# Kernel tuning notes

Measured on AMD Instinct MI355X. Metric: run time of the kernel, lower is better.

Reference implementation:

```python
import jax, jax.numpy as jnp
import numpy as np

B, W, K = 262144, 8, 3      # batch of triples, context window, negatives per item
V, E = 100000, 128          # vocab, embedding dim


def setup_inputs() -> dict:
    key = jax.random.key(0)
    k1, k2, k3, k4, k5 = jax.random.split(key, 5)
    targets = jax.random.randint(k1, (B,), 0, V)
    contexts = jax.random.randint(k2, (B, W), 0, V)
    negsamples = jax.random.randint(k3, (B, K), 0, V)
    # learned params (small random so the loss/grads are non-degenerate)
    target_W = jax.random.normal(k4, (V, E), dtype=jnp.float32) * 0.01
    context_W = jax.random.normal(k5, (V, E), dtype=jnp.float32) * 0.01
    return {"targets": targets, "contexts": contexts, "negsamples": negsamples,
            "target_W": target_W, "context_W": context_W}


def reference(targets, contexts, negsamples, target_W, context_W):
    tgt = target_W[targets]                      # [B,E] one target embedding per triple
    ctx = context_W[contexts].mean(axis=1)       # [B,E] mean of context window embeddings
    neg = context_W[negsamples]                  # [B,K,E] negative-sample context embeddings
    pos_score = jnp.einsum('be,be->b', ctx, tgt)             # [B]
    neg_score = -jnp.einsum('bke,be->b', neg, tgt)           # [B] sum_k dot(-neg_k, tgt)
    per_item = jax.nn.log_sigmoid(pos_score) + jax.nn.log_sigmoid(neg_score)
    return -per_item.mean()                      # scalar NEG loss (sum over items / B)
```

## Files before the change

kernel.cpp:

```cpp
#include <hip/hip_runtime.h>
#include <math.h>
#include <stdint.h>

#define B_ITEMS 262144
#define W_CTX   8
#define K_NEG   3
#define E_DIM   128
#define V_VOCAB 100000

typedef _Float16 half_t;
typedef __attribute__((ext_vector_type(2))) _Float16 half2_t;

#define F16_TABLE_BYTES ((size_t)V_VOCAB * E_DIM * 2)

__device__ __forceinline__ float log_sigmoid_f(float x) {
    return fminf(x, 0.0f) - log1pf(expf(-fabsf(x)));
}

__device__ __forceinline__ float dot2acc(half2_t a, half2_t b, float c) {
#if __has_builtin(__builtin_amdgcn_fdot2)
    return __builtin_amdgcn_fdot2(a, b, c, false);
#else
    return c + (float)a[0] * (float)b[0] + (float)a[1] * (float)b[1];
#endif
}

__device__ __forceinline__ half2_t h2_from_u32(uint32_t u) {
    return __builtin_bit_cast(half2_t, u);
}
__device__ __forceinline__ uint32_t u32_from_h2(half2_t h) {
    return __builtin_bit_cast(uint32_t, h);
}

__global__ void init_out_kernel(float* out) {
    if (threadIdx.x == 0 && blockIdx.x == 0) out[0] = 0.0f;
}

__global__ void __launch_bounds__(256) convert_f16_both_kernel(
    const float* __restrict__ srcA, uint2* __restrict__ dstA,
    const float* __restrict__ srcB, uint2* __restrict__ dstB, int n4)
{
    int i = blockIdx.x * blockDim.x + threadIdx.x;
    const int stride = gridDim.x * blockDim.x;
    const float4* a4 = reinterpret_cast<const float4*>(srcA);
    const float4* b4 = reinterpret_cast<const float4*>(srcB);
    for (; i < n4; i += stride) {
        float4 va = a4[i];
        uint2 oa;
        oa.x = u32_from_h2(half2_t{(half_t)va.x, (half_t)va.y});
        oa.y = u32_from_h2(half2_t{(half_t)va.z, (half_t)va.w});
        dstA[i] = oa;
        if (dstB) {
            float4 vb = b4[i];
            uint2 ob;
            ob.x = u32_from_h2(half2_t{(half_t)vb.x, (half_t)vb.y});
            ob.y = u32_from_h2(half2_t{(half_t)vb.z, (half_t)vb.w});
            dstB[i] = ob;
        }
    }
}

template <bool CTX16, bool TGT16>
__global__ void __launch_bounds__(256, 8) cbow_kernel(
    const int*      __restrict__ targets,
    const int*      __restrict__ contexts,
    const int*      __restrict__ negsamples,
    const float*    __restrict__ target_W,
    const float*    __restrict__ context_W,
    const uint32_t* __restrict__ ctx16,
    const uint32_t* __restrict__ tgt16,
    float*          __restrict__ out)
{
    const int lane = threadIdx.x & 63;
    const int wib  = threadIdx.x >> 6;
    const int wid  = blockIdx.x * (blockDim.x >> 6) + wib;
    const int grp  = lane >> 4;
    const int sub  = lane & 15;
    const uint32_t sub16 = (uint32_t)sub * 16;

    const char* ctxb = reinterpret_cast<const char*>(ctx16);
    const char* tgtb = reinterpret_cast<const char*>(tgt16);

    float wave_sum = 0.0f;

    for (int i = 0; i < 8; ++i) {
        const int b = (wid * 8 + i) * 4 + grp;

        const int4 c0 = *reinterpret_cast<const int4*>(&contexts[b * W_CTX]);
        const int4 c1 = *reinterpret_cast<const int4*>(&contexts[b * W_CTX + 4]);
        const int  n0 = negsamples[b * K_NEG + 0];
        const int  n1 = negsamples[b * K_NEG + 1];
        const int  n2 = negsamples[b * K_NEG + 2];
        const int  t  = targets[b];

        half2_t tg[4];
        if constexpr (TGT16) {
            const uint4 tv = *reinterpret_cast<const uint4*>(
                tgtb + (((uint32_t)t) << 8) + sub16);
            tg[0] = h2_from_u32(tv.x); tg[1] = h2_from_u32(tv.y);
            tg[2] = h2_from_u32(tv.z); tg[3] = h2_from_u32(tv.w);
        } else {
            const float4 f0 = *reinterpret_cast<const float4*>(
                &target_W[(size_t)t * E_DIM + sub * 8]);
            const float4 f1 = *reinterpret_cast<const float4*>(
                &target_W[(size_t)t * E_DIM + sub * 8 + 4]);
            tg[0] = half2_t{(half_t)f0.x, (half_t)f0.y};
            tg[1] = half2_t{(half_t)f0.z, (half_t)f0.w};
            tg[2] = half2_t{(half_t)f1.x, (half_t)f1.y};
            tg[3] = half2_t{(half_t)f1.z, (half_t)f1.w};
        }

        float p0 = 0.f, p1 = 0.f, p2 = 0.f, p3 = 0.f;
        float q0 = 0.f, q1 = 0.f, q2 = 0.f, q3 = 0.f;

        auto row = [&](int idx, float& a0, float& a1, float& a2, float& a3) {
            if constexpr (CTX16) {
                const uint4 rv = *reinterpret_cast<const uint4*>(
                    ctxb + (((uint32_t)idx) << 8) + sub16);
                a0 = dot2acc(h2_from_u32(rv.x), tg[0], a0);
                a1 = dot2acc(h2_from_u32(rv.y), tg[1], a1);
                a2 = dot2acc(h2_from_u32(rv.z), tg[2], a2);
                a3 = dot2acc(h2_from_u32(rv.w), tg[3], a3);
            } else {
                const float4 f0 = *reinterpret_cast<const float4*>(
                    &context_W[(size_t)idx * E_DIM + sub * 8]);
                const float4 f1 = *reinterpret_cast<const float4*>(
                    &context_W[(size_t)idx * E_DIM + sub * 8 + 4]);
                a0 = dot2acc(half2_t{(half_t)f0.x, (half_t)f0.y}, tg[0], a0);
                a1 = dot2acc(half2_t{(half_t)f0.z, (half_t)f0.w}, tg[1], a1);
                a2 = dot2acc(half2_t{(half_t)f1.x, (half_t)f1.y}, tg[2], a2);
                a3 = dot2acc(half2_t{(half_t)f1.z, (half_t)f1.w}, tg[3], a3);
            }
        };

        row(c0.x, p0, p1, p2, p3);
        row(c0.y, p0, p1, p2, p3);
        row(c0.z, p0, p1, p2, p3);
        row(c0.w, p0, p1, p2, p3);
        row(c1.x, p0, p1, p2, p3);
        row(c1.y, p0, p1, p2, p3);
        row(c1.z, p0, p1, p2, p3);
        row(c1.w, p0, p1, p2, p3);
        row(n0,   q0, q1, q2, q3);
        row(n1,   q0, q1, q2, q3);
        row(n2,   q0, q1, q2, q3);

        float pos = (p0 + p1) + (p2 + p3);
        float neg = (q0 + q1) + (q2 + q3);

        #pragma unroll
        for (int off = 8; off > 0; off >>= 1) {
            pos += __shfl_xor(pos, off, 64);
            neg += __shfl_xor(neg, off, 64);
        }

        wave_sum += log_sigmoid_f(pos * (1.0f / W_CTX)) + log_sigmoid_f(-neg);
    }

    wave_sum += __shfl_xor(wave_sum, 16, 64);
    wave_sum += __shfl_xor(wave_sum, 32, 64);

    __shared__ float sm[4];
    if (lane == 0) sm[wib] = wave_sum;
    __syncthreads();
    if (threadIdx.x == 0) {
        atomicAdd(out, (sm[0] + sm[1] + sm[2] + sm[3]) * (-1.0f / (float)B_ITEMS));
    }
}

extern "C" void kernel_launch(void* const* d_in, const int* in_sizes, int n_in,
                              void* d_out, int out_size, void* d_ws, size_t ws_size,
                              hipStream_t stream) {
    const int*   targets    = (const int*)  d_in[0];
    const int*   contexts   = (const int*)  d_in[1];
    const int*   negsamples = (const int*)  d_in[2];
    const float* target_W   = (const float*)d_in[3];
    const float* context_W  = (const float*)d_in[4];
    float*       out        = (float*)      d_out;

    init_out_kernel<<<1, 64, 0, stream>>>(out);

    uint32_t* ctx16 = (uint32_t*)d_ws;
    uint32_t* tgt16 = (uint32_t*)((char*)d_ws + F16_TABLE_BYTES);
    const int n4 = V_VOCAB * E_DIM / 4;

    if (ws_size >= 2 * F16_TABLE_BYTES) {
        convert_f16_both_kernel<<<2048, 256, 0, stream>>>(
            context_W, (uint2*)ctx16, target_W, (uint2*)tgt16, n4);
        cbow_kernel<true, true><<<2048, 256, 0, stream>>>(
            targets, contexts, negsamples, target_W, context_W, ctx16, tgt16, out);
    } else if (ws_size >= F16_TABLE_BYTES) {
        convert_f16_both_kernel<<<2048, 256, 0, stream>>>(
            context_W, (uint2*)ctx16, nullptr, (uint2*)nullptr, n4);
        cbow_kernel<true, false><<<2048, 256, 0, stream>>>(
            targets, contexts, negsamples, target_W, context_W, ctx16, nullptr, out);
    } else {
        cbow_kernel<false, false><<<2048, 256, 0, stream>>>(
            targets, contexts, negsamples, target_W, context_W, nullptr, nullptr, out);
    }
}
```

Before: 240.9 us.

## Store context table as FP8 and gather half-size rows in the CBOW kernel

```diff
diff --git a/kernel.cpp b/kernel.cpp
--- a/kernel.cpp
+++ b/kernel.cpp
@@ -10,21 +10,21 @@
 
 typedef _Float16 half_t;
 typedef __attribute__((ext_vector_type(2))) _Float16 half2_t;
-
+typedef __attribute__((ext_vector_type(2))) float   fvec2;
+
+#define CTX_FP8_BYTES ((size_t)V_VOCAB * E_DIM)
 #define F16_TABLE_BYTES ((size_t)V_VOCAB * E_DIM * 2)
+
+#if __has_builtin(__builtin_amdgcn_cvt_pk_f32_fp8) && __has_builtin(__builtin_amdgcn_cvt_pk_fp8_f32)
+#define HAVE_FP8 1
+#else
+#define HAVE_FP8 0
+#endif
 
 __device__ __forceinline__ float log_sigmoid_f(float x) {
     return fminf(x, 0.0f) - log1pf(expf(-fabsf(x)));
 }
 
-__device__ __forceinline__ float dot2acc(half2_t a, half2_t b, float c) {
-#if __has_builtin(__builtin_amdgcn_fdot2)
-    return __builtin_amdgcn_fdot2(a, b, c, false);
-#else
-    return c + (float)a[0] * (float)b[0] + (float)a[1] * (float)b[1];
-#endif
-}
-
 __device__ __forceinline__ half2_t h2_from_u32(uint32_t u) {
     return __builtin_bit_cast(half2_t, u);
 }
@@ -36,10 +36,41 @@
     if (threadIdx.x == 0 && blockIdx.x == 0) out[0] = 0.0f;
 }
 
+#if HAVE_FP8
+__global__ void __launch_bounds__(256) convert_fp8_kernel(
+    const float* __restrict__ ctx, uint2* __restrict__ ctx8,
+    const float* __restrict__ tgt, uint4* __restrict__ tgt16,
+    int n8, float* __restrict__ out)
+{
+    if (blockIdx.x == 0 && threadIdx.x == 0) out[0] = 0.0f;
+    int i = blockIdx.x * blockDim.x + threadIdx.x;
+    const int stride = gridDim.x * blockDim.x;
+    const float4* c4 = reinterpret_cast<const float4*>(ctx);
+    const float4* t4 = reinterpret_cast<const float4*>(tgt);
+    for (; i < n8; i += stride) {
+        float4 a = c4[2 * i], b = c4[2 * i + 1];
+        int lo = __builtin_amdgcn_cvt_pk_fp8_f32(a.x, a.y, 0, false);
+        lo     = __builtin_amdgcn_cvt_pk_fp8_f32(a.z, a.w, lo, true);
+        int hi = __builtin_amdgcn_cvt_pk_fp8_f32(b.x, b.y, 0, false);
+        hi     = __builtin_amdgcn_cvt_pk_fp8_f32(b.z, b.w, hi, true);
+        ctx8[i] = make_uint2((uint32_t)lo, (uint32_t)hi);
+        float4 ta = t4[2 * i], tb = t4[2 * i + 1];
+        uint4 o;
+        o.x = u32_from_h2(half2_t{(half_t)ta.x, (half_t)ta.y});
+        o.y = u32_from_h2(half2_t{(half_t)ta.z, (half_t)ta.w});
+        o.z = u32_from_h2(half2_t{(half_t)tb.x, (half_t)tb.y});
+        o.w = u32_from_h2(half2_t{(half_t)tb.z, (half_t)tb.w});
+        tgt16[i] = o;
+    }
+}
+#endif
+
 __global__ void __launch_bounds__(256) convert_f16_both_kernel(
     const float* __restrict__ srcA, uint2* __restrict__ dstA,
-    const float* __restrict__ srcB, uint2* __restrict__ dstB, int n4)
+    const float* __restrict__ srcB, uint2* __restrict__ dstB,
+    int n4, float* __restrict__ out)
 {
+    if (blockIdx.x == 0 && threadIdx.x == 0) out[0] = 0.0f;
     int i = blockIdx.x * blockDim.x + threadIdx.x;
     const int stride = gridDim.x * blockDim.x;
     const float4* a4 = reinterpret_cast<const float4*>(srcA);
@@ -50,25 +81,24 @@
         oa.x = u32_from_h2(half2_t{(half_t)va.x, (half_t)va.y});
         oa.y = u32_from_h2(half2_t{(half_t)va.z, (half_t)va.w});
         dstA[i] = oa;
-        if (dstB) {
-            float4 vb = b4[i];
-            uint2 ob;
-            ob.x = u32_from_h2(half2_t{(half_t)vb.x, (half_t)vb.y});
-            ob.y = u32_from_h2(half2_t{(half_t)vb.z, (half_t)vb.w});
-            dstB[i] = ob;
-        }
-    }
-}
-
-template <bool CTX16, bool TGT16>
+        float4 vb = b4[i];
+        uint2 ob;
+        ob.x = u32_from_h2(half2_t{(half_t)vb.x, (half_t)vb.y});
+        ob.y = u32_from_h2(half2_t{(half_t)vb.z, (half_t)vb.w});
+        dstB[i] = ob;
+    }
+}
+
+template <int MODE>
 __global__ void __launch_bounds__(256, 8) cbow_kernel(
     const int*      __restrict__ targets,
     const int*      __restrict__ contexts,
     const int*      __restrict__ negsamples,
     const float*    __restrict__ target_W,
     const float*    __restrict__ context_W,
-    const uint32_t* __restrict__ ctx16,
-    const uint32_t* __restrict__ tgt16,
+    const char*     __restrict__ ctx8,
+    const char*     __restrict__ ctx16,
+    const char*     __restrict__ tgt16,
     float*          __restrict__ out)
 {
     const int lane = threadIdx.x & 63;
@@ -76,15 +106,12 @@
     const int wid  = blockIdx.x * (blockDim.x >> 6) + wib;
     const int grp  = lane >> 4;
     const int sub  = lane & 15;
-    const uint32_t sub16 = (uint32_t)sub * 16;
-
-    const char* ctxb = reinterpret_cast<const char*>(ctx16);
-    const char* tgtb = reinterpret_cast<const char*>(tgt16);
 
     float wave_sum = 0.0f;
 
-    for (int i = 0; i < 8; ++i) {
-        const int b = (wid * 8 + i) * 4 + grp;
+    #pragma unroll
+    for (int i = 0; i < 4; ++i) {
+        const int b = wid * 16 + i * 4 + grp;
 
         const int4 c0 = *reinterpret_cast<const int4*>(&contexts[b * W_CTX]);
         const int4 c1 = *reinterpret_cast<const int4*>(&contexts[b * W_CTX + 4]);
@@ -93,43 +120,63 @@
         const int  n2 = negsamples[b * K_NEG + 2];
         const int  t  = targets[b];
 
+        float   tf[8];
         half2_t tg[4];
-        if constexpr (TGT16) {
-            const uint4 tv = *reinterpret_cast<const uint4*>(
-                tgtb + (((uint32_t)t) << 8) + sub16);
-            tg[0] = h2_from_u32(tv.x); tg[1] = h2_from_u32(tv.y);
-            tg[2] = h2_from_u32(tv.z); tg[3] = h2_from_u32(tv.w);
-        } else {
+        if constexpr (MODE == 0) {
             const float4 f0 = *reinterpret_cast<const float4*>(
                 &target_W[(size_t)t * E_DIM + sub * 8]);
             const float4 f1 = *reinterpret_cast<const float4*>(
                 &target_W[(size_t)t * E_DIM + sub * 8 + 4]);
-            tg[0] = half2_t{(half_t)f0.x, (half_t)f0.y};
-            tg[1] = half2_t{(half_t)f0.z, (half_t)f0.w};
-            tg[2] = half2_t{(half_t)f1.x, (half_t)f1.y};
-            tg[3] = half2_t{(half_t)f1.z, (half_t)f1.w};
+            tf[0]=f0.x; tf[1]=f0.y; tf[2]=f0.z; tf[3]=f0.w;
+            tf[4]=f1.x; tf[5]=f1.y; tf[6]=f1.z; tf[7]=f1.w;
+        } else {
+            const uint4 tv = *reinterpret_cast<const uint4*>(
+                tgt16 + (((uint32_t)t) << 8) + sub * 16);
+            if constexpr (MODE == 1) {
+                tg[0] = h2_from_u32(tv.x); tg[1] = h2_from_u32(tv.y);
+                tg[2] = h2_from_u32(tv.z); tg[3] = h2_from_u32(tv.w);
+            } else {
+                half2_t h;
+                h = h2_from_u32(tv.x); tf[0] = (float)h[0]; tf[1] = (float)h[1];
+                h = h2_from_u32(tv.y); tf[2] = (float)h[0]; tf[3] = (float)h[1];
+                h = h2_from_u32(tv.z); tf[4] = (float)h[0]; tf[5] = (float)h[1];
+                h = h2_from_u32(tv.w); tf[6] = (float)h[0]; tf[7] = (float)h[1];
+            }
         }
 
         float p0 = 0.f, p1 = 0.f, p2 = 0.f, p3 = 0.f;
         float q0 = 0.f, q1 = 0.f, q2 = 0.f, q3 = 0.f;
 
         auto row = [&](int idx, float& a0, float& a1, float& a2, float& a3) {
-            if constexpr (CTX16) {
+            if constexpr (MODE == 2) {
+#if HAVE_FP8
+                const uint2 rv = *reinterpret_cast<const uint2*>(
+                    ctx8 + (((uint32_t)idx) << 7) + sub * 8);
+                const fvec2 d0 = __builtin_amdgcn_cvt_pk_f32_fp8((int)rv.x, false);
+                const fvec2 d1 = __builtin_amdgcn_cvt_pk_f32_fp8((int)rv.x, true);
+                const fvec2 d2 = __builtin_amdgcn_cvt_pk_f32_fp8((int)rv.y, false);
+                const fvec2 d3 = __builtin_amdgcn_cvt_pk_f32_fp8((int)rv.y, true);
+                a0 += d0.x * tf[0] + d0.y * tf[1];
+                a1 += d1.x * tf[2] + d1.y * tf[3];
+                a2 += d2.x * tf[4] + d2.y * tf[5];
+                a3 += d3.x * tf[6] + d3.y * tf[7];
+#endif
+            } else if constexpr (MODE == 1) {
                 const uint4 rv = *reinterpret_cast<const uint4*>(
-                    ctxb + (((uint32_t)idx) << 8) + sub16);
-                a0 = dot2acc(h2_from_u32(rv.x), tg[0], a0);
-                a1 = dot2acc(h2_from_u32(rv.y), tg[1], a1);
-                a2 = dot2acc(h2_from_u32(rv.z), tg[2], a2);
-                a3 = dot2acc(h2_from_u32(rv.w), tg[3], a3);
+                    ctx16 + (((uint32_t)idx) << 8) + sub * 16);
+                a0 = __builtin_amdgcn_fdot2(h2_from_u32(rv.x), tg[0], a0, false);
+                a1 = __builtin_amdgcn_fdot2(h2_from_u32(rv.y), tg[1], a1, false);
+                a2 = __builtin_amdgcn_fdot2(h2_from_u32(rv.z), tg[2], a2, false);
+                a3 = __builtin_amdgcn_fdot2(h2_from_u32(rv.w), tg[3], a3, false);
             } else {
                 const float4 f0 = *reinterpret_cast<const float4*>(
                     &context_W[(size_t)idx * E_DIM + sub * 8]);
                 const float4 f1 = *reinterpret_cast<const float4*>(
                     &context_W[(size_t)idx * E_DIM + sub * 8 + 4]);
-                a0 = dot2acc(half2_t{(half_t)f0.x, (half_t)f0.y}, tg[0], a0);
-                a1 = dot2acc(half2_t{(half_t)f0.z, (half_t)f0.w}, tg[1], a1);
-                a2 = dot2acc(half2_t{(half_t)f1.x, (half_t)f1.y}, tg[2], a2);
-                a3 = dot2acc(half2_t{(half_t)f1.z, (half_t)f1.w}, tg[3], a3);
+                a0 += f0.x * tf[0] + f0.y * tf[1];
+                a1 += f0.z * tf[2] + f0.w * tf[3];
+                a2 += f1.x * tf[4] + f1.y * tf[5];
+                a3 += f1.z * tf[6] + f1.w * tf[7];
             }
         };
 
@@ -178,24 +225,34 @@
     const float* context_W  = (const float*)d_in[4];
     float*       out        = (float*)      d_out;
 
-    init_out_kernel<<<1, 64, 0, stream>>>(out);
-
-    uint32_t* ctx16 = (uint32_t*)d_ws;
-    uint32_t* tgt16 = (uint32_t*)((char*)d_ws + F16_TABLE_BYTES);
-    const int n4 = V_VOCAB * E_DIM / 4;
-
+    const int blocks = 4096, threads = 256;
+
+#if HAVE_FP8
+    if (ws_size >= CTX_FP8_BYTES + F16_TABLE_BYTES) {
+        char* ctx8  = (char*)d_ws;
+        char* tgt16 = (char*)d_ws + CTX_FP8_BYTES;
+        const int n8 = V_VOCAB * E_DIM / 8;
+        convert_fp8_kernel<<<2048, 256, 0, stream>>>(
+            context_W, (uint2*)ctx8, target_W, (uint4*)tgt16, n8, out);
+        cbow_kernel<2><<<blocks, threads, 0, stream>>>(
+            targets, contexts, negsamples, target_W, context_W,
+            ctx8, nullptr, tgt16, out);
+        return;
+    }
+#endif
     if (ws_size >= 2 * F16_TABLE_BYTES) {
+        char* ctx16 = (char*)d_ws;
+        char* tgt16 = (char*)d_ws + F16_TABLE_BYTES;
+        const int n4 = V_VOCAB * E_DIM / 4;
         convert_f16_both_kernel<<<2048, 256, 0, stream>>>(
-            context_W, (uint2*)ctx16, target_W, (uint2*)tgt16, n4);
-        cbow_kernel<true, true><<<2048, 256, 0, stream>>>(
-            targets, contexts, negsamples, target_W, context_W, ctx16, tgt16, out);
-    } else if (ws_size >= F16_TABLE_BYTES) {
-        convert_f16_both_kernel<<<2048, 256, 0, stream>>>(
-            context_W, (uint2*)ctx16, nullptr, (uint2*)nullptr, n4);
-        cbow_kernel<true, false><<<2048, 256, 0, stream>>>(
-            targets, contexts, negsamples, target_W, context_W, ctx16, nullptr, out);
+            context_W, (uint2*)ctx16, target_W, (uint2*)tgt16, n4, out);
+        cbow_kernel<1><<<blocks, threads, 0, stream>>>(
+            targets, contexts, negsamples, target_W, context_W,
+            nullptr, ctx16, tgt16, out);
     } else {
-        cbow_kernel<false, false><<<2048, 256, 0, stream>>>(
-            targets, contexts, negsamples, target_W, context_W, nullptr, nullptr, out);
-    }
-}
+        init_out_kernel<<<1, 64, 0, stream>>>(out);
+        cbow_kernel<0><<<blocks, threads, 0, stream>>>(
+            targets, contexts, negsamples, target_W, context_W,
+            nullptr, nullptr, nullptr, out);
+    }
+}
```

Result: no change. 240.4 us (-0.2%).
